# Kernel tuning notes

Measured on AMD Instinct MI355X. Metric: run time of the kernel, lower is better.

The kernel has to match this reference:

```python
import jax, jax.numpy as jnp
import numpy as np

TOPK = 0.1  # fraction of h*w spatial positions, from __init__ default


def setup_inputs() -> dict:
    key = jax.random.key(0)
    x = jax.random.normal(key, (32, 256, 56, 56), dtype=jnp.float32)
    return {"x": x}


def reference(x) -> jnp.ndarray:
    # Faithful translation of TopKLayer.sparse_hw (including its quirky
    # comparison of ascending *ranks* against the spatial *index* of the
    # k-th largest element, exactly as the torch code does).
    n, c, h, w = x.shape
    k = int(max(1, TOPK * h * w))  # topk_keep_num = 313 for 56x56
    x_r = x.reshape(n * c, h * w)              # (nc, hw)
    abs_x = jnp.abs(x_r)
    # ranks[i, j] = ascending rank of abs_x[i, j] within row i
    ranks = jnp.argsort(jnp.argsort(abs_x, axis=1), axis=1)
    # spatial index of the k-th largest |x| in each row
    thr_idx = jax.lax.top_k(abs_x, k)[1][:, -1]  # (nc,)
    mask = (ranks < thr_idx[:, None]).reshape(n, c, h, w)
    return x * mask.astype(x.dtype)
```

## Files before the change

kernel.cpp:

```cpp
#include <hip/hip_runtime.h>
#include <stdint.h>


#define HW    3136
#define NT    128
#define KSEL  313u
#define CAP   320u
#define CAP2  64u
#define O_CAND 0
#define O_HC   384
#define O_TINY 704
#define M31   0x7fffffffu
#define SENT  0xFFFFFFFFu

__device__ __forceinline__ unsigned wscan_incl(unsigned v) {
    const int lane = threadIdx.x & 63;
#pragma unroll
    for (int d = 1; d < 64; d <<= 1) {
        unsigned o = __shfl_up(v, d, 64);
        if (lane >= d) v += o;
    }
    return v;
}

__device__ __forceinline__ unsigned bcast_first(unsigned flag, unsigned val) {
    unsigned long long bal = __ballot(flag != 0);
    if (!bal) return 0u;
    return __shfl(val, __ffsll(bal) - 1, 64);
}

__device__ __forceinline__ void hadd(unsigned* h, unsigned b) {
    atomicAdd(&h[b >> 1], (b & 1) ? 0x10000u : 1u);
}

template <bool fromTop>
__device__ void wave_finish(unsigned* hr, unsigned* br) {
    const int lane = threadIdx.x & 63;
    const unsigned cnt = br[3];
    const unsigned m1  = br[1];
    unsigned* cand = hr + O_CAND;
    unsigned* hc   = hr + O_HC;
    unsigned* tiny = hr + O_TINY;
    if (cnt > CAP) { if (lane == 0) br[2] = (m1 == 0) ? 0u : SENT; return; }
    for (unsigned i = lane; i < cnt; i += 64) atomicAdd(&hc[cand[i] >> 24], 1u);
    unsigned hh[4];
#pragma unroll
    for (int i = 0; i < 4; ++i) hh[i] = hc[4 * lane + i];
    const unsigned s4 = hh[0] + hh[1] + hh[2] + hh[3];
    unsigned run2 = wscan_incl(s4) - s4;
    unsigned packed2 = 0;
#pragma unroll
    for (int i = 0; i < 4; ++i) {
        if (fromTop) {
            const unsigned suf = cnt - run2 - hh[i];
            if (suf < m1 && m1 <= suf + hh[i])
                packed2 = ((unsigned)(4 * lane + i) << 16) | (m1 - suf);
        } else {
            if (run2 < m1 && m1 <= run2 + hh[i])
                packed2 = ((unsigned)(4 * lane + i) << 16) | (m1 - run2);
        }
        run2 += hh[i];
    }
    packed2 = bcast_first(packed2, packed2);
    if (packed2 == 0) { if (lane == 0) br[2] = 0u; return; }
    const unsigned b2 = packed2 >> 16;
    const unsigned m2 = packed2 & 0xFFFFu;
    unsigned tc = 0;
    for (unsigned i = lane; i < cnt; i += 64) tc += ((cand[i] >> 24) == b2);
    const unsigned tincl = wscan_incl(tc);
    const unsigned c2 = __shfl((int)tincl, 63, 64);
    if (c2 > CAP2) { if (lane == 0) br[2] = SENT; return; }
    unsigned tpos = tincl - tc;
    for (unsigned i = lane; i < cnt; i += 64) {
        const unsigned cw = cand[i];
        if ((cw >> 24) == b2) tiny[tpos++] = cw;
    }
    unsigned hitf = 0, resv = 0;
    if ((unsigned)lane < c2) {
        const unsigned ci = tiny[lane];
        const unsigned di = fromTop ? (ci ^ 0xFFFu) : ci;
        unsigned r = 1;
        for (unsigned j = 0; j < c2; ++j) {
            const unsigned dj = fromTop ? (tiny[j] ^ 0xFFFu) : tiny[j];
            if (fromTop ? (dj > di) : (dj < di)) r++;
        }
        if (r == m2) { hitf = 1; resv = ci; }
    }
    resv = bcast_first(hitf, resv);
    if (lane == 0) br[2] = resv;
}

template <bool fromTop>
__device__ void block_fallback(const unsigned* __restrict__ gx, unsigned* br) {
    const unsigned b0 = br[0], m1 = br[1];
    const int t = threadIdx.x;
    for (int j = t; j < HW; j += NT) {
        const unsigned k = gx[j] & M31;
        if ((k >> 20) != b0) continue;
        unsigned Ci = ((k & 0xFFFFFu) << 12) | (unsigned)j;
        if (fromTop) Ci ^= 0xFFFu;
        unsigned r = 1;
        for (int j2 = 0; j2 < HW; ++j2) {
            const unsigned k2 = gx[j2] & M31;
            if ((k2 >> 20) != b0) continue;
            unsigned Cj = ((k2 & 0xFFFFFu) << 12) | (unsigned)j2;
            if (fromTop) Cj ^= 0xFFFu;
            if (fromTop ? (Cj > Ci) : (Cj < Ci)) r++;
        }
        if (r == m1) br[2] = ((k & 0xFFFFFu) << 12) | (unsigned)j;
    }
}

extern "C" __global__ void __launch_bounds__(NT, 6)
topk_kernel(const float* __restrict__ x, float* __restrict__ out) {
    __shared__ unsigned s_h[1024];
    __shared__ unsigned s_warp[2];
    __shared__ unsigned s_b[4];

    const int t = threadIdx.x;
    const int lane = t & 63;
    const int wid = t >> 6;
    const size_t row = blockIdx.x;
    const uint4* __restrict__ xin = (const uint4*)(x + row * HW);
    uint4* __restrict__ xo = (uint4*)(out + row * HW);
    const unsigned* __restrict__ gx = (const unsigned*)xin;
    const uint4 z4 = make_uint4(0u, 0u, 0u, 0u);

    uint4 v[6];
#pragma unroll
    for (int i = 0; i < 6; ++i) v[i] = xin[t + NT * i];
    uint4 vt = (t < 16) ? xin[768 + t] : z4;
#pragma unroll
    for (int i = 0; i < 6; ++i)
        asm volatile("" : "+v"(v[i].x), "+v"(v[i].y), "+v"(v[i].z), "+v"(v[i].w));
    asm volatile("" : "+v"(vt.x), "+v"(vt.y), "+v"(vt.z), "+v"(vt.w));

    ((uint4*)s_h)[t] = z4;
    ((uint4*)s_h)[t + NT] = z4;
    __syncthreads();

#pragma unroll
    for (int i = 0; i < 6; ++i) {
        hadd(s_h, (v[i].x & M31) >> 20); hadd(s_h, (v[i].y & M31) >> 20);
        hadd(s_h, (v[i].z & M31) >> 20); hadd(s_h, (v[i].w & M31) >> 20);
    }
    if (t < 16) {
        hadd(s_h, (vt.x & M31) >> 20); hadd(s_h, (vt.y & M31) >> 20);
        hadd(s_h, (vt.z & M31) >> 20); hadd(s_h, (vt.w & M31) >> 20);
    }
    __syncthreads();

    const uint4 w0 = ((const uint4*)s_h)[2 * t];
    const uint4 w1 = ((const uint4*)s_h)[2 * t + 1];
    unsigned cpk[8] = {w0.x, w0.y, w0.z, w0.w, w1.x, w1.y, w1.z, w1.w};
    unsigned ssum = 0;
#pragma unroll
    for (int j = 0; j < 8; ++j) ssum += (cpk[j] & 0xFFFFu) + (cpk[j] >> 16);
    const unsigned Si = wscan_incl(ssum);
    if (lane == 63) s_warp[wid] = Si;
    __syncthreads();

    const unsigned base = Si - ssum + (wid ? s_warp[0] : 0u);
    {
        unsigned run = base;
#pragma unroll
        for (int j = 0; j < 8; ++j) {
            const unsigned lo = cpk[j] & 0xFFFFu, hi = cpk[j] >> 16;
            unsigned suf = HW - run - lo;
            if (suf < KSEL && KSEL <= suf + lo) { s_b[0] = 16u * t + 2u * j; s_b[1] = KSEL - suf; }
            run += lo;
            suf = HW - run - hi;
            if (suf < KSEL && KSEL <= suf + hi) { s_b[0] = 16u * t + 2u * j + 1u; s_b[1] = KSEL - suf; }
            run += hi;
        }
    }
    if (t == 0) s_b[3] = 0;
    s_h[O_HC + t] = 0; s_h[O_HC + t + NT] = 0;
    __syncthreads();

    auto compact_regs = [&](unsigned b0) {
        auto cput = [&](unsigned wv, unsigned idx) {
            const unsigned k = wv & M31;
            if ((k >> 20) == b0) {
                const unsigned p = atomicAdd(&s_b[3], 1u);
                if (p < CAP) s_h[O_CAND + p] = ((k & 0xFFFFFu) << 12) | idx;
            }
        };
#pragma unroll
        for (int i = 0; i < 6; ++i) {
            const unsigned i0 = 4u * (unsigned)(t + NT * i);
            cput(v[i].x, i0); cput(v[i].y, i0 + 1u);
            cput(v[i].z, i0 + 2u); cput(v[i].w, i0 + 3u);
        }
        if (t < 16) {
            const unsigned i0 = 4u * (unsigned)(768 + t);
            cput(vt.x, i0); cput(vt.y, i0 + 1u);
            cput(vt.z, i0 + 2u); cput(vt.w, i0 + 3u);
        }
    };
    compact_regs(s_b[0]);
    __syncthreads();

    if (wid == 0) wave_finish<true>(s_h, s_b);
    __syncthreads();

    unsigned compA = s_b[2];
    if (compA == SENT) { block_fallback<true>(gx, s_b); __syncthreads(); compA = s_b[2]; }
    const unsigned tIdx = compA & 0xFFFu;

    {
        unsigned run = base;
#pragma unroll
        for (int j = 0; j < 8; ++j) {
            const unsigned lo = cpk[j] & 0xFFFFu, hi = cpk[j] >> 16;
            if (run < tIdx && tIdx <= run + lo) { s_b[0] = 16u * t + 2u * j; s_b[1] = tIdx - run; }
            run += lo;
            if (run < tIdx && tIdx <= run + hi) { s_b[0] = 16u * t + 2u * j + 1u; s_b[1] = tIdx - run; }
            run += hi;
        }
    }
    if (t == 0) {
        s_b[3] = 0;
        if (tIdx == 0) { s_b[0] = 0; s_b[1] = 0; }
    }
    s_h[O_HC + t] = 0; s_h[O_HC + t + NT] = 0;
    __syncthreads();

    const unsigned b0B = s_b[0];
    compact_regs(b0B);
    __syncthreads();

    if (wid == 0) wave_finish<false>(s_h, s_b);
    __syncthreads();

    unsigned compB = s_b[2];
    if (compB == SENT) { block_fallback<false>(gx, s_b); __syncthreads(); compB = s_b[2]; }
    const unsigned KB = (b0B << 20) | (compB >> 12);
    const unsigned eB = compB & 0xFFFu;

    {
        auto msk = [&](unsigned wv, unsigned idx) -> unsigned {
            const unsigned k = wv & M31;
            return (k < KB || (k == KB && idx <= eB)) ? wv : 0u;
        };
#pragma unroll
        for (int i = 0; i < 6; ++i) {
            const unsigned i0 = 4u * (unsigned)(t + NT * i);
            uint4 o = v[i];
            o.x = msk(o.x, i0); o.y = msk(o.y, i0 + 1u);
            o.z = msk(o.z, i0 + 2u); o.w = msk(o.w, i0 + 3u);
            xo[t + NT * i] = o;
        }
        if (t < 16) {
            const unsigned i0 = 4u * (unsigned)(768 + t);
            uint4 o = vt;
            o.x = msk(o.x, i0); o.y = msk(o.y, i0 + 1u);
            o.z = msk(o.z, i0 + 2u); o.w = msk(o.w, i0 + 3u);
            xo[768 + t] = o;
        }
    }
}

extern "C" void kernel_launch(void* const* d_in, const int* in_sizes, int n_in,
                              void* d_out, int out_size, void* d_ws, size_t ws_size,
                              hipStream_t stream) {
    const float* x = (const float*)d_in[0];
    float* out = (float*)d_out;
    const int rows = in_sizes[0] / HW;
    topk_kernel<<<dim3(rows), dim3(NT), 0, stream>>>(x, out);
}
```

Before: 59.61 us.

## Let each wave scan the full histogram to remove block barriers

Each wave now loads and scans the whole 2048-bin packed histogram (stored with padding against bank conflicts) so it can find the threshold bucket by itself. This removes the cross-wave scan exchange and several __syncthreads per row. Candidate compaction uses per-wave segments and counters to reduce atomic contention, and the launch bound moves to 8 blocks per SIMD. The trade-off is redundant per-wave scan work (16 words per lane), higher register pressure, and a lower per-wave candidate cap that sends more rows to the slow fallback path.

```diff
diff --git a/kernel.cpp b/kernel.cpp
--- a/kernel.cpp
+++ b/kernel.cpp
@@ -5,13 +5,18 @@
 #define HW    3136
 #define NT    128
 #define KSEL  313u
-#define CAP   320u
+#define CAPH  256u
 #define CAP2  64u
-#define O_CAND 0
-#define O_HC   384
-#define O_TINY 704
 #define M31   0x7fffffffu
 #define SENT  0xFFFFFFFFu
+
+#define O_H    0
+#define O_CAND 1088
+#define O_HC   1600
+#define O_TINY 1856
+#define O_CNT  1920
+#define O_RES  1922
+#define LDSW   1924
 
 __device__ __forceinline__ unsigned wscan_incl(unsigned v) {
     const int lane = threadIdx.x & 63;
@@ -30,19 +35,53 @@
 }
 
 __device__ __forceinline__ void hadd(unsigned* h, unsigned b) {
-    atomicAdd(&h[b >> 1], (b & 1) ? 0x10000u : 1u);
+    const unsigned w = b >> 1;
+    atomicAdd(&h[w + (w >> 4)], (b & 1) ? 0x10000u : 1u);
 }
 
 template <bool fromTop>
-__device__ void wave_finish(unsigned* hr, unsigned* br) {
+__device__ __forceinline__ unsigned locate2048(const unsigned* pc, unsigned base,
+                                               unsigned rank) {
     const int lane = threadIdx.x & 63;
-    const unsigned cnt = br[3];
-    const unsigned m1  = br[1];
-    unsigned* cand = hr + O_CAND;
-    unsigned* hc   = hr + O_HC;
-    unsigned* tiny = hr + O_TINY;
-    if (cnt > CAP) { if (lane == 0) br[2] = (m1 == 0) ? 0u : SENT; return; }
-    for (unsigned i = lane; i < cnt; i += 64) atomicAdd(&hc[cand[i] >> 24], 1u);
+    unsigned run = base, packed = 0;
+#pragma unroll
+    for (int j = 0; j < 16; ++j) {
+        const unsigned lo = pc[j] & 0xFFFFu, hi = pc[j] >> 16;
+        if (fromTop) {
+            unsigned suf = HW - run - lo;
+            if (suf < rank && rank <= suf + lo)
+                packed = ((32u * lane + 2u * j) << 16) | (rank - suf);
+            run += lo;
+            suf = HW - run - hi;
+            if (suf < rank && rank <= suf + hi)
+                packed = ((32u * lane + 2u * j + 1u) << 16) | (rank - suf);
+            run += hi;
+        } else {
+            if (run < rank && rank <= run + lo)
+                packed = ((32u * lane + 2u * j) << 16) | (rank - run);
+            run += lo;
+            if (run < rank && rank <= run + hi)
+                packed = ((32u * lane + 2u * j + 1u) << 16) | (rank - run);
+            run += hi;
+        }
+    }
+    return bcast_first(packed, packed);
+}
+
+template <bool fromTop>
+__device__ unsigned wave_finish(unsigned* lds, unsigned m1) {
+    const int lane = threadIdx.x & 63;
+    unsigned* cand = lds + O_CAND;
+    unsigned* hc   = lds + O_HC;
+    unsigned* tiny = lds + O_TINY;
+    const unsigned c0 = lds[O_CNT], c1 = lds[O_CNT + 1];
+    if (m1 == 0) return 0u;
+    if (c0 > CAPH || c1 > CAPH) return SENT;
+    const unsigned cnt = c0 + c1;
+#pragma unroll
+    for (int i = 0; i < 4; ++i) hc[lane + 64 * i] = 0;
+    for (unsigned i = lane; i < c0; i += 64) atomicAdd(&hc[cand[i] >> 24], 1u);
+    for (unsigned i = lane; i < c1; i += 64) atomicAdd(&hc[cand[CAPH + i] >> 24], 1u);
     unsigned hh[4];
 #pragma unroll
     for (int i = 0; i < 4; ++i) hh[i] = hc[4 * lane + i];
@@ -62,17 +101,22 @@
         run2 += hh[i];
     }
     packed2 = bcast_first(packed2, packed2);
-    if (packed2 == 0) { if (lane == 0) br[2] = 0u; return; }
+    if (packed2 == 0) return 0u;
     const unsigned b2 = packed2 >> 16;
     const unsigned m2 = packed2 & 0xFFFFu;
     unsigned tc = 0;
-    for (unsigned i = lane; i < cnt; i += 64) tc += ((cand[i] >> 24) == b2);
+    for (unsigned i = lane; i < c0; i += 64) tc += ((cand[i] >> 24) == b2);
+    for (unsigned i = lane; i < c1; i += 64) tc += ((cand[CAPH + i] >> 24) == b2);
     const unsigned tincl = wscan_incl(tc);
     const unsigned c2 = __shfl((int)tincl, 63, 64);
-    if (c2 > CAP2) { if (lane == 0) br[2] = SENT; return; }
+    if (c2 > CAP2) return SENT;
     unsigned tpos = tincl - tc;
-    for (unsigned i = lane; i < cnt; i += 64) {
+    for (unsigned i = lane; i < c0; i += 64) {
         const unsigned cw = cand[i];
+        if ((cw >> 24) == b2) tiny[tpos++] = cw;
+    }
+    for (unsigned i = lane; i < c1; i += 64) {
+        const unsigned cw = cand[CAPH + i];
         if ((cw >> 24) == b2) tiny[tpos++] = cw;
     }
     unsigned hitf = 0, resv = 0;
@@ -86,13 +130,12 @@
         }
         if (r == m2) { hitf = 1; resv = ci; }
     }
-    resv = bcast_first(hitf, resv);
-    if (lane == 0) br[2] = resv;
+    return bcast_first(hitf, resv);
 }
 
 template <bool fromTop>
-__device__ void block_fallback(const unsigned* __restrict__ gx, unsigned* br) {
-    const unsigned b0 = br[0], m1 = br[1];
+__device__ void block_fallback(const unsigned* __restrict__ gx,
+                               unsigned b0, unsigned m1, unsigned* res) {
     const int t = threadIdx.x;
     for (int j = t; j < HW; j += NT) {
         const unsigned k = gx[j] & M31;
@@ -107,15 +150,13 @@
             if (fromTop) Cj ^= 0xFFFu;
             if (fromTop ? (Cj > Ci) : (Cj < Ci)) r++;
         }
-        if (r == m1) br[2] = ((k & 0xFFFFFu) << 12) | (unsigned)j;
-    }
-}
-
-extern "C" __global__ void __launch_bounds__(NT, 6)
+        if (r == m1) res[0] = ((k & 0xFFFFFu) << 12) | (unsigned)j;
+    }
+}
+
+extern "C" __global__ void __launch_bounds__(NT, 8)
 topk_kernel(const float* __restrict__ x, float* __restrict__ out) {
-    __shared__ unsigned s_h[1024];
-    __shared__ unsigned s_warp[2];
-    __shared__ unsigned s_b[4];
+    __shared__ unsigned lds[LDSW];
 
     const int t = threadIdx.x;
     const int lane = t & 63;
@@ -135,55 +176,38 @@
         asm volatile("" : "+v"(v[i].x), "+v"(v[i].y), "+v"(v[i].z), "+v"(v[i].w));
     asm volatile("" : "+v"(vt.x), "+v"(vt.y), "+v"(vt.z), "+v"(vt.w));
 
-    ((uint4*)s_h)[t] = z4;
-    ((uint4*)s_h)[t + NT] = z4;
+    for (int i = t; i < 1088; i += NT) lds[O_H + i] = 0;
     __syncthreads();
 
 #pragma unroll
     for (int i = 0; i < 6; ++i) {
-        hadd(s_h, (v[i].x & M31) >> 20); hadd(s_h, (v[i].y & M31) >> 20);
-        hadd(s_h, (v[i].z & M31) >> 20); hadd(s_h, (v[i].w & M31) >> 20);
+        hadd(lds, (v[i].x & M31) >> 20); hadd(lds, (v[i].y & M31) >> 20);
+        hadd(lds, (v[i].z & M31) >> 20); hadd(lds, (v[i].w & M31) >> 20);
     }
     if (t < 16) {
-        hadd(s_h, (vt.x & M31) >> 20); hadd(s_h, (vt.y & M31) >> 20);
-        hadd(s_h, (vt.z & M31) >> 20); hadd(s_h, (vt.w & M31) >> 20);
-    }
-    __syncthreads();
-
-    const uint4 w0 = ((const uint4*)s_h)[2 * t];
-    const uint4 w1 = ((const uint4*)s_h)[2 * t + 1];
-    unsigned cpk[8] = {w0.x, w0.y, w0.z, w0.w, w1.x, w1.y, w1.z, w1.w};
+        hadd(lds, (vt.x & M31) >> 20); hadd(lds, (vt.y & M31) >> 20);
+        hadd(lds, (vt.z & M31) >> 20); hadd(lds, (vt.w & M31) >> 20);
+    }
+    __syncthreads();
+
+    unsigned pc[16];
+#pragma unroll
+    for (int j = 0; j < 16; ++j) pc[j] = lds[O_H + 17 * lane + j];
     unsigned ssum = 0;
 #pragma unroll
-    for (int j = 0; j < 8; ++j) ssum += (cpk[j] & 0xFFFFu) + (cpk[j] >> 16);
-    const unsigned Si = wscan_incl(ssum);
-    if (lane == 63) s_warp[wid] = Si;
-    __syncthreads();
-
-    const unsigned base = Si - ssum + (wid ? s_warp[0] : 0u);
-    {
-        unsigned run = base;
-#pragma unroll
-        for (int j = 0; j < 8; ++j) {
-            const unsigned lo = cpk[j] & 0xFFFFu, hi = cpk[j] >> 16;
-            unsigned suf = HW - run - lo;
-            if (suf < KSEL && KSEL <= suf + lo) { s_b[0] = 16u * t + 2u * j; s_b[1] = KSEL - suf; }
-            run += lo;
-            suf = HW - run - hi;
-            if (suf < KSEL && KSEL <= suf + hi) { s_b[0] = 16u * t + 2u * j + 1u; s_b[1] = KSEL - suf; }
-            run += hi;
-        }
-    }
-    if (t == 0) s_b[3] = 0;
-    s_h[O_HC + t] = 0; s_h[O_HC + t + NT] = 0;
-    __syncthreads();
-
+    for (int j = 0; j < 16; ++j) ssum += (pc[j] & 0xFFFFu) + (pc[j] >> 16);
+    const unsigned base = wscan_incl(ssum) - ssum;
+    const unsigned pA = locate2048<true>(pc, base, KSEL);
+    const unsigned b0A = pA >> 16, m1A = pA & 0xFFFFu;
+
+    unsigned* cseg = lds + O_CAND + wid * CAPH;
+    unsigned* cctr = lds + O_CNT + wid;
     auto compact_regs = [&](unsigned b0) {
         auto cput = [&](unsigned wv, unsigned idx) {
             const unsigned k = wv & M31;
             if ((k >> 20) == b0) {
-                const unsigned p = atomicAdd(&s_b[3], 1u);
-                if (p < CAP) s_h[O_CAND + p] = ((k & 0xFFFFFu) << 12) | idx;
+                const unsigned p = atomicAdd(cctr, 1u);
+                if (p < CAPH) cseg[p] = ((k & 0xFFFFFu) << 12) | idx;
             }
         };
 #pragma unroll
@@ -198,43 +222,43 @@
             cput(vt.z, i0 + 2u); cput(vt.w, i0 + 3u);
         }
     };
-    compact_regs(s_b[0]);
-    __syncthreads();
-
-    if (wid == 0) wave_finish<true>(s_h, s_b);
-    __syncthreads();
-
-    unsigned compA = s_b[2];
-    if (compA == SENT) { block_fallback<true>(gx, s_b); __syncthreads(); compA = s_b[2]; }
+    if (lane == 0) *cctr = 0;
+    compact_regs(b0A);
+    __syncthreads();
+
+    if (wid == 0) {
+        const unsigned r = wave_finish<true>(lds, m1A);
+        if (lane == 0) lds[O_RES] = r;
+    }
+    __syncthreads();
+    unsigned compA = lds[O_RES];
+    if (compA == SENT) {
+        block_fallback<true>(gx, b0A, m1A, lds + O_RES);
+        __syncthreads();
+        compA = lds[O_RES];
+    }
     const unsigned tIdx = compA & 0xFFFu;
 
-    {
-        unsigned run = base;
-#pragma unroll
-        for (int j = 0; j < 8; ++j) {
-            const unsigned lo = cpk[j] & 0xFFFFu, hi = cpk[j] >> 16;
-            if (run < tIdx && tIdx <= run + lo) { s_b[0] = 16u * t + 2u * j; s_b[1] = tIdx - run; }
-            run += lo;
-            if (run < tIdx && tIdx <= run + hi) { s_b[0] = 16u * t + 2u * j + 1u; s_b[1] = tIdx - run; }
-            run += hi;
-        }
-    }
-    if (t == 0) {
-        s_b[3] = 0;
-        if (tIdx == 0) { s_b[0] = 0; s_b[1] = 0; }
-    }
-    s_h[O_HC + t] = 0; s_h[O_HC + t + NT] = 0;
-    __syncthreads();
-
-    const unsigned b0B = s_b[0];
+#pragma unroll
+    for (int j = 0; j < 16; ++j) pc[j] = lds[O_H + 17 * lane + j];
+    const unsigned pB = locate2048<false>(pc, base, tIdx);
+    const unsigned b0B = pB >> 16, m1B = pB & 0xFFFFu;
+
+    if (lane == 0) *cctr = 0;
     compact_regs(b0B);
     __syncthreads();
 
-    if (wid == 0) wave_finish<false>(s_h, s_b);
-    __syncthreads();
-
-    unsigned compB = s_b[2];
-    if (compB == SENT) { block_fallback<false>(gx, s_b); __syncthreads(); compB = s_b[2]; }
+    if (wid == 0) {
+        const unsigned r = wave_finish<false>(lds, m1B);
+        if (lane == 0) lds[O_RES] = r;
+    }
+    __syncthreads();
+    unsigned compB = lds[O_RES];
+    if (compB == SENT) {
+        block_fallback<false>(gx, b0B, m1B, lds + O_RES);
+        __syncthreads();
+        compB = lds[O_RES];
+    }
     const unsigned KB = (b0B << 20) | (compB >> 12);
     const unsigned eB = compB & 0xFFFu;
 
```

Result: slower. 107.0 us (+79.6%).

## Use 256 threads per row block with padded LDS histogram layout

Applied to the files above, without the earlier changes.

Doubles the block size from 128 to 256 threads, so each thread holds 3 uint4 vectors plus a tail instead of 6, and rewrites the histogram scan for 4 waves. The histogram is padded by one word every 16 to reduce LDS bank conflicts on atomic adds and scan reads. Selection parameters are passed in registers instead of re-read from shared memory. The intent is more parallelism per row and less register pressure. The cost is extra cross-wave synchronisation, and launch_bounds(256,6) may limit occupancy.

```diff
diff --git a/kernel.cpp b/kernel.cpp
--- a/kernel.cpp
+++ b/kernel.cpp
@@ -3,15 +3,18 @@
 
 
 #define HW    3136
-#define NT    128
+#define NT    256
 #define KSEL  313u
 #define CAP   320u
 #define CAP2  64u
-#define O_CAND 0
-#define O_HC   384
-#define O_TINY 704
 #define M31   0x7fffffffu
 #define SENT  0xFFFFFFFFu
+
+#define O_H    0
+#define O_CAND 1088
+#define O_HC   1408
+#define O_TINY 1664
+#define LDSW   1728
 
 __device__ __forceinline__ unsigned wscan_incl(unsigned v) {
     const int lane = threadIdx.x & 63;
@@ -30,18 +33,18 @@
 }
 
 __device__ __forceinline__ void hadd(unsigned* h, unsigned b) {
-    atomicAdd(&h[b >> 1], (b & 1) ? 0x10000u : 1u);
+    const unsigned w = b >> 1;
+    atomicAdd(&h[w + (w >> 4)], (b & 1) ? 0x10000u : 1u);
 }
 
 template <bool fromTop>
-__device__ void wave_finish(unsigned* hr, unsigned* br) {
+__device__ unsigned wave_finish(unsigned* lds, unsigned m1, unsigned cnt) {
     const int lane = threadIdx.x & 63;
-    const unsigned cnt = br[3];
-    const unsigned m1  = br[1];
-    unsigned* cand = hr + O_CAND;
-    unsigned* hc   = hr + O_HC;
-    unsigned* tiny = hr + O_TINY;
-    if (cnt > CAP) { if (lane == 0) br[2] = (m1 == 0) ? 0u : SENT; return; }
+    unsigned* cand = lds + O_CAND;
+    unsigned* hc   = lds + O_HC;
+    unsigned* tiny = lds + O_TINY;
+    if (m1 == 0) return 0u;
+    if (cnt > CAP) return SENT;
     for (unsigned i = lane; i < cnt; i += 64) atomicAdd(&hc[cand[i] >> 24], 1u);
     unsigned hh[4];
 #pragma unroll
@@ -62,14 +65,14 @@
         run2 += hh[i];
     }
     packed2 = bcast_first(packed2, packed2);
-    if (packed2 == 0) { if (lane == 0) br[2] = 0u; return; }
+    if (packed2 == 0) return 0u;
     const unsigned b2 = packed2 >> 16;
     const unsigned m2 = packed2 & 0xFFFFu;
     unsigned tc = 0;
     for (unsigned i = lane; i < cnt; i += 64) tc += ((cand[i] >> 24) == b2);
     const unsigned tincl = wscan_incl(tc);
     const unsigned c2 = __shfl((int)tincl, 63, 64);
-    if (c2 > CAP2) { if (lane == 0) br[2] = SENT; return; }
+    if (c2 > CAP2) return SENT;
     unsigned tpos = tincl - tc;
     for (unsigned i = lane; i < cnt; i += 64) {
         const unsigned cw = cand[i];
@@ -86,13 +89,12 @@
         }
         if (r == m2) { hitf = 1; resv = ci; }
     }
-    resv = bcast_first(hitf, resv);
-    if (lane == 0) br[2] = resv;
+    return bcast_first(hitf, resv);
 }
 
 template <bool fromTop>
-__device__ void block_fallback(const unsigned* __restrict__ gx, unsigned* br) {
-    const unsigned b0 = br[0], m1 = br[1];
+__device__ void block_fallback(const unsigned* __restrict__ gx,
+                               unsigned b0, unsigned m1, unsigned* res) {
     const int t = threadIdx.x;
     for (int j = t; j < HW; j += NT) {
         const unsigned k = gx[j] & M31;
@@ -107,14 +109,14 @@
             if (fromTop) Cj ^= 0xFFFu;
             if (fromTop ? (Cj > Ci) : (Cj < Ci)) r++;
         }
-        if (r == m1) br[2] = ((k & 0xFFFFFu) << 12) | (unsigned)j;
+        if (r == m1) res[0] = ((k & 0xFFFFFu) << 12) | (unsigned)j;
     }
 }
 
 extern "C" __global__ void __launch_bounds__(NT, 6)
 topk_kernel(const float* __restrict__ x, float* __restrict__ out) {
-    __shared__ unsigned s_h[1024];
-    __shared__ unsigned s_warp[2];
+    __shared__ unsigned lds[LDSW];
+    __shared__ unsigned s_warp[4];
     __shared__ unsigned s_b[4];
 
     const int t = threadIdx.x;
@@ -125,57 +127,67 @@
     uint4* __restrict__ xo = (uint4*)(out + row * HW);
     const unsigned* __restrict__ gx = (const unsigned*)xin;
     const uint4 z4 = make_uint4(0u, 0u, 0u, 0u);
-
-    uint4 v[6];
-#pragma unroll
-    for (int i = 0; i < 6; ++i) v[i] = xin[t + NT * i];
-    uint4 vt = (t < 16) ? xin[768 + t] : z4;
-#pragma unroll
-    for (int i = 0; i < 6; ++i)
-        asm volatile("" : "+v"(v[i].x), "+v"(v[i].y), "+v"(v[i].z), "+v"(v[i].w));
+    const bool tail = (t < 16);
+
+    uint4 v0 = xin[t];
+    uint4 v1 = xin[t + NT];
+    uint4 v2 = xin[t + 2 * NT];
+    uint4 vt = tail ? xin[768 + t] : z4;
+    asm volatile("" : "+v"(v0.x), "+v"(v0.y), "+v"(v0.z), "+v"(v0.w));
+    asm volatile("" : "+v"(v1.x), "+v"(v1.y), "+v"(v1.z), "+v"(v1.w));
+    asm volatile("" : "+v"(v2.x), "+v"(v2.y), "+v"(v2.z), "+v"(v2.w));
     asm volatile("" : "+v"(vt.x), "+v"(vt.y), "+v"(vt.z), "+v"(vt.w));
 
-    ((uint4*)s_h)[t] = z4;
-    ((uint4*)s_h)[t + NT] = z4;
-    __syncthreads();
-
-#pragma unroll
-    for (int i = 0; i < 6; ++i) {
-        hadd(s_h, (v[i].x & M31) >> 20); hadd(s_h, (v[i].y & M31) >> 20);
-        hadd(s_h, (v[i].z & M31) >> 20); hadd(s_h, (v[i].w & M31) >> 20);
-    }
-    if (t < 16) {
-        hadd(s_h, (vt.x & M31) >> 20); hadd(s_h, (vt.y & M31) >> 20);
-        hadd(s_h, (vt.z & M31) >> 20); hadd(s_h, (vt.w & M31) >> 20);
-    }
-    __syncthreads();
-
-    const uint4 w0 = ((const uint4*)s_h)[2 * t];
-    const uint4 w1 = ((const uint4*)s_h)[2 * t + 1];
-    unsigned cpk[8] = {w0.x, w0.y, w0.z, w0.w, w1.x, w1.y, w1.z, w1.w};
+    {
+        uint4* h4 = (uint4*)(lds + O_H);
+        h4[t] = z4;
+        if (tail) h4[NT + t] = z4;
+    }
+    __syncthreads();
+
+    hadd(lds, (v0.x & M31) >> 20); hadd(lds, (v0.y & M31) >> 20);
+    hadd(lds, (v0.z & M31) >> 20); hadd(lds, (v0.w & M31) >> 20);
+    hadd(lds, (v1.x & M31) >> 20); hadd(lds, (v1.y & M31) >> 20);
+    hadd(lds, (v1.z & M31) >> 20); hadd(lds, (v1.w & M31) >> 20);
+    hadd(lds, (v2.x & M31) >> 20); hadd(lds, (v2.y & M31) >> 20);
+    hadd(lds, (v2.z & M31) >> 20); hadd(lds, (v2.w & M31) >> 20);
+    if (tail) {
+        hadd(lds, (vt.x & M31) >> 20); hadd(lds, (vt.y & M31) >> 20);
+        hadd(lds, (vt.z & M31) >> 20); hadd(lds, (vt.w & M31) >> 20);
+    }
+    __syncthreads();
+
+    unsigned cpk[4];
+    {
+        const unsigned a0 = 4u * (unsigned)t + ((unsigned)t >> 2);
+#pragma unroll
+        for (int j = 0; j < 4; ++j) cpk[j] = lds[O_H + a0 + j];
+    }
     unsigned ssum = 0;
 #pragma unroll
-    for (int j = 0; j < 8; ++j) ssum += (cpk[j] & 0xFFFFu) + (cpk[j] >> 16);
+    for (int j = 0; j < 4; ++j) ssum += (cpk[j] & 0xFFFFu) + (cpk[j] >> 16);
     const unsigned Si = wscan_incl(ssum);
     if (lane == 63) s_warp[wid] = Si;
     __syncthreads();
 
-    const unsigned base = Si - ssum + (wid ? s_warp[0] : 0u);
+    unsigned cross = 0;
+    for (int w2 = 0; w2 < wid; ++w2) cross += s_warp[w2];
+    const unsigned base = cross + Si - ssum;
     {
         unsigned run = base;
 #pragma unroll
-        for (int j = 0; j < 8; ++j) {
+        for (int j = 0; j < 4; ++j) {
             const unsigned lo = cpk[j] & 0xFFFFu, hi = cpk[j] >> 16;
             unsigned suf = HW - run - lo;
-            if (suf < KSEL && KSEL <= suf + lo) { s_b[0] = 16u * t + 2u * j; s_b[1] = KSEL - suf; }
+            if (suf < KSEL && KSEL <= suf + lo) { s_b[0] = 8u * t + 2u * j; s_b[1] = KSEL - suf; }
             run += lo;
             suf = HW - run - hi;
-            if (suf < KSEL && KSEL <= suf + hi) { s_b[0] = 16u * t + 2u * j + 1u; s_b[1] = KSEL - suf; }
+            if (suf < KSEL && KSEL <= suf + hi) { s_b[0] = 8u * t + 2u * j + 1u; s_b[1] = KSEL - suf; }
             run += hi;
         }
     }
     if (t == 0) s_b[3] = 0;
-    s_h[O_HC + t] = 0; s_h[O_HC + t + NT] = 0;
+    lds[O_HC + t] = 0;
     __syncthreads();
 
     auto compact_regs = [&](unsigned b0) {
@@ -183,39 +195,46 @@
             const unsigned k = wv & M31;
             if ((k >> 20) == b0) {
                 const unsigned p = atomicAdd(&s_b[3], 1u);
-                if (p < CAP) s_h[O_CAND + p] = ((k & 0xFFFFFu) << 12) | idx;
+                if (p < CAP) lds[O_CAND + p] = ((k & 0xFFFFFu) << 12) | idx;
             }
         };
-#pragma unroll
-        for (int i = 0; i < 6; ++i) {
-            const unsigned i0 = 4u * (unsigned)(t + NT * i);
-            cput(v[i].x, i0); cput(v[i].y, i0 + 1u);
-            cput(v[i].z, i0 + 2u); cput(v[i].w, i0 + 3u);
-        }
-        if (t < 16) {
-            const unsigned i0 = 4u * (unsigned)(768 + t);
-            cput(vt.x, i0); cput(vt.y, i0 + 1u);
-            cput(vt.z, i0 + 2u); cput(vt.w, i0 + 3u);
+        unsigned i0 = 4u * (unsigned)t;
+        cput(v0.x, i0); cput(v0.y, i0 + 1u); cput(v0.z, i0 + 2u); cput(v0.w, i0 + 3u);
+        i0 = 4u * (unsigned)(t + NT);
+        cput(v1.x, i0); cput(v1.y, i0 + 1u); cput(v1.z, i0 + 2u); cput(v1.w, i0 + 3u);
+        i0 = 4u * (unsigned)(t + 2 * NT);
+        cput(v2.x, i0); cput(v2.y, i0 + 1u); cput(v2.z, i0 + 2u); cput(v2.w, i0 + 3u);
+        if (tail) {
+            i0 = 4u * (unsigned)(768 + t);
+            cput(vt.x, i0); cput(vt.y, i0 + 1u); cput(vt.z, i0 + 2u); cput(vt.w, i0 + 3u);
         }
     };
-    compact_regs(s_b[0]);
-    __syncthreads();
-
-    if (wid == 0) wave_finish<true>(s_h, s_b);
-    __syncthreads();
-
+    const unsigned b0A = s_b[0];
+    const unsigned m1A = s_b[1];
+    compact_regs(b0A);
+    __syncthreads();
+
+    if (wid == 0) {
+        const unsigned r = wave_finish<true>(lds, m1A, s_b[3]);
+        if (lane == 0) s_b[2] = r;
+    }
+    __syncthreads();
     unsigned compA = s_b[2];
-    if (compA == SENT) { block_fallback<true>(gx, s_b); __syncthreads(); compA = s_b[2]; }
+    if (compA == SENT) {
+        block_fallback<true>(gx, b0A, m1A, &s_b[2]);
+        __syncthreads();
+        compA = s_b[2];
+    }
     const unsigned tIdx = compA & 0xFFFu;
 
     {
         unsigned run = base;
 #pragma unroll
-        for (int j = 0; j < 8; ++j) {
+        for (int j = 0; j < 4; ++j) {
             const unsigned lo = cpk[j] & 0xFFFFu, hi = cpk[j] >> 16;
-            if (run < tIdx && tIdx <= run + lo) { s_b[0] = 16u * t + 2u * j; s_b[1] = tIdx - run; }
+            if (run < tIdx && tIdx <= run + lo) { s_b[0] = 8u * t + 2u * j; s_b[1] = tIdx - run; }
             run += lo;
-            if (run < tIdx && tIdx <= run + hi) { s_b[0] = 16u * t + 2u * j + 1u; s_b[1] = tIdx - run; }
+            if (run < tIdx && tIdx <= run + hi) { s_b[0] = 8u * t + 2u * j + 1u; s_b[1] = tIdx - run; }
             run += hi;
         }
     }
@@ -223,18 +242,25 @@
         s_b[3] = 0;
         if (tIdx == 0) { s_b[0] = 0; s_b[1] = 0; }
     }
-    s_h[O_HC + t] = 0; s_h[O_HC + t + NT] = 0;
+    lds[O_HC + t] = 0;
     __syncthreads();
 
     const unsigned b0B = s_b[0];
+    const unsigned m1B = s_b[1];
     compact_regs(b0B);
     __syncthreads();
 
-    if (wid == 0) wave_finish<false>(s_h, s_b);
-    __syncthreads();
-
+    if (wid == 0) {
+        const unsigned r = wave_finish<false>(lds, m1B, s_b[3]);
+        if (lane == 0) s_b[2] = r;
+    }
+    __syncthreads();
     unsigned compB = s_b[2];
-    if (compB == SENT) { block_fallback<false>(gx, s_b); __syncthreads(); compB = s_b[2]; }
+    if (compB == SENT) {
+        block_fallback<false>(gx, b0B, m1B, &s_b[2]);
+        __syncthreads();
+        compB = s_b[2];
+    }
     const unsigned KB = (b0B << 20) | (compB >> 12);
     const unsigned eB = compB & 0xFFFu;
 
@@ -243,19 +269,23 @@
             const unsigned k = wv & M31;
             return (k < KB || (k == KB && idx <= eB)) ? wv : 0u;
         };
-#pragma unroll
-        for (int i = 0; i < 6; ++i) {
-            const unsigned i0 = 4u * (unsigned)(t + NT * i);
-            uint4 o = v[i];
-            o.x = msk(o.x, i0); o.y = msk(o.y, i0 + 1u);
-            o.z = msk(o.z, i0 + 2u); o.w = msk(o.w, i0 + 3u);
-            xo[t + NT * i] = o;
-        }
-        if (t < 16) {
-            const unsigned i0 = 4u * (unsigned)(768 + t);
-            uint4 o = vt;
-            o.x = msk(o.x, i0); o.y = msk(o.y, i0 + 1u);
-            o.z = msk(o.z, i0 + 2u); o.w = msk(o.w, i0 + 3u);
+        uint4 o;
+        unsigned i0 = 4u * (unsigned)t;
+        o.x = msk(v0.x, i0); o.y = msk(v0.y, i0 + 1u);
+        o.z = msk(v0.z, i0 + 2u); o.w = msk(v0.w, i0 + 3u);
+        xo[t] = o;
+        i0 = 4u * (unsigned)(t + NT);
+        o.x = msk(v1.x, i0); o.y = msk(v1.y, i0 + 1u);
+        o.z = msk(v1.z, i0 + 2u); o.w = msk(v1.w, i0 + 3u);
+        xo[t + NT] = o;
+        i0 = 4u * (unsigned)(t + 2 * NT);
+        o.x = msk(v2.x, i0); o.y = msk(v2.y, i0 + 1u);
+        o.z = msk(v2.z, i0 + 2u); o.w = msk(v2.w, i0 + 3u);
+        xo[t + 2 * NT] = o;
+        if (tail) {
+            i0 = 4u * (unsigned)(768 + t);
+            o.x = msk(vt.x, i0); o.y = msk(vt.y, i0 + 1u);
+            o.z = msk(vt.z, i0 + 2u); o.w = msk(vt.w, i0 + 3u);
             xo[768 + t] = o;
         }
     }
```

New measurement: 70.04 us. 1.17x slower.
